# Kernel tuning notes

Measured on AMD Instinct MI355X. Metric: run time of the kernel, lower is better.

The kernel has to match this reference:

```python
import jax, jax.numpy as jnp
import numpy as np

SIGMA = 20.0  # outlier threshold used by FindOutliers
EPS = 1e-8


def setup_inputs() -> dict:
    key = jax.random.key(0)
    k1, k2, k3 = jax.random.split(key, 3)
    B, S, K, N = 2, 2048, 4096, 4096
    x = jax.random.normal(k1, (B, S, K), jnp.float32)
    # inject 8 outlier feature columns (|x| > sigma) so the fp correction path is exercised
    out_cols = jnp.arange(8) * (K // 8)
    x = x.at[:, :, out_cols].multiply(30.0)
    weight = jax.random.normal(k2, (N, K), jnp.float32) * (1.0 / np.sqrt(K))
    bias = jax.random.normal(k3, (N,), jnp.float32) * 0.01
    return {"x": x, "weight": weight, "bias": bias}


def reference(x, weight, bias):
    # x: [B,S,K], weight: [N,K], bias: [N]
    B, S, K = x.shape
    N = weight.shape[0]
    xf = x.reshape(-1, K)  # [M,K]

    # FindOutliers: columns where any activation exceeds sigma (as a fixed-size mask)
    col_mask = jnp.any(jnp.abs(xf) > SIGMA, axis=0)          # [K] bool
    keep = jnp.logical_not(col_mask)

    # weight quantization: zero outlier columns, per-output-row symmetric int8
    w_in = weight * keep[None, :].astype(weight.dtype)        # [N,K]
    q_scale = jnp.max(jnp.abs(w_in), axis=1) / 127.0          # [N]
    q_scale = jnp.maximum(q_scale, EPS)
    q_w = jnp.round(jnp.clip(w_in / q_scale[:, None], -128.0, 127.0)).astype(jnp.int8)

    # per-token (row) activation quantization (FindRowScaleF32)
    row_scale = jnp.max(jnp.abs(xf), axis=1, keepdims=True) / 127.0  # [M,1] fp32
    row_scale = jnp.maximum(row_scale, EPS)
    q_x = jnp.round(jnp.clip(xf / row_scale, -128.0, 127.0)).astype(jnp.int8)

    # int8 GEMM with int32 accumulation, then dequant + bias
    acc = jnp.matmul(q_x.astype(jnp.int32), q_w.T.astype(jnp.int32)).astype(jnp.float32)  # [M,N]
    y = acc * row_scale * q_scale[None, :]

    # fp outlier correction: x[:, ind] @ weight[:, ind].T  (dense masked form, same math)
    x_out = xf * col_mask[None, :].astype(xf.dtype)
    y = y + x_out @ weight.T

    y = y + bias[None, :]
    return y.reshape(B, S, N)
```

## Files before the change

kernel.cpp:

```cpp
#include <hip/hip_runtime.h>
#include <stdint.h>

#define K_DIM 4096
#define N_DIM 4096
#define SIGMA 20.0f
#define EPSQ 1e-8f

typedef __attribute__((ext_vector_type(4))) int i32x4;

#define GLDS16(gp, lp)                                                         \
  __builtin_amdgcn_global_load_lds(                                            \
      (const __attribute__((address_space(1))) unsigned int*)(const void*)(gp),\
      (__attribute__((address_space(3))) unsigned int*)(void*)(lp), 16, 0, 0)

__global__ __launch_bounds__(256) void k_rowquant(
    const float* __restrict__ x, float* __restrict__ row_scale,
    int* __restrict__ mask, int8_t* __restrict__ qx)
{
  const int wave = threadIdx.x >> 6;
  const int lane = threadIdx.x & 63;
  const int m = blockIdx.x * 4 + wave;
  const float4* xr = (const float4*)(x + (size_t)m * K_DIM);
  float4 v[16];
  float amax = 0.0f;
#pragma unroll
  for (int c = 0; c < 16; ++c) {
    v[c] = xr[lane + c * 64];
    float a0 = fabsf(v[c].x), a1 = fabsf(v[c].y);
    float a2 = fabsf(v[c].z), a3 = fabsf(v[c].w);
    amax = fmaxf(amax, fmaxf(fmaxf(a0, a1), fmaxf(a2, a3)));
    int kb = (lane + c * 64) * 4;
    if (a0 > SIGMA) mask[kb + 0] = 1;
    if (a1 > SIGMA) mask[kb + 1] = 1;
    if (a2 > SIGMA) mask[kb + 2] = 1;
    if (a3 > SIGMA) mask[kb + 3] = 1;
  }
#pragma unroll
  for (int off = 32; off > 0; off >>= 1)
    amax = fmaxf(amax, __shfl_xor(amax, off, 64));
  const float rs = fmaxf(amax / 127.0f, EPSQ);
  if (lane == 0) row_scale[m] = rs;
  uint32_t* qxo = (uint32_t*)(qx + (size_t)m * K_DIM);
#pragma unroll
  for (int c = 0; c < 16; ++c) {
    int q0 = (int)rintf(fminf(fmaxf(v[c].x / rs, -128.0f), 127.0f));
    int q1 = (int)rintf(fminf(fmaxf(v[c].y / rs, -128.0f), 127.0f));
    int q2 = (int)rintf(fminf(fmaxf(v[c].z / rs, -128.0f), 127.0f));
    int q3 = (int)rintf(fminf(fmaxf(v[c].w / rs, -128.0f), 127.0f));
    qxo[lane + c * 64] = (uint32_t)(q0 & 0xff) | ((uint32_t)(q1 & 0xff) << 8) |
                         ((uint32_t)(q2 & 0xff) << 16) | ((uint32_t)(q3 & 0xff) << 24);
  }
}

__global__ __launch_bounds__(256) void k_wquant(
    const float* __restrict__ w, const int* __restrict__ mask,
    float* __restrict__ q_scale, int8_t* __restrict__ qw,
    int* __restrict__ outlist, int* __restrict__ count)
{
  if (blockIdx.x == 0) {
    __shared__ int lcnt;
    if (threadIdx.x == 0) lcnt = 0;
    __syncthreads();
    for (int k = threadIdx.x; k < K_DIM; k += 256)
      if (mask[k] == 1) { int i = atomicAdd(&lcnt, 1); outlist[i] = k; }
    __syncthreads();
    if (threadIdx.x == 0) *count = lcnt;
  }

  const int wave = threadIdx.x >> 6;
  const int lane = threadIdx.x & 63;
  const int n = blockIdx.x * 4 + wave;
  const float4* wr = (const float4*)(w + (size_t)n * K_DIM);
  const int4* mr = (const int4*)mask;
  float4 v[16];
  float amax = 0.0f;
#pragma unroll
  for (int c = 0; c < 16; ++c) {
    float4 vv = wr[lane + c * 64];
    int4 mm = mr[lane + c * 64];
    vv.x = (mm.x == 1) ? 0.0f : vv.x;
    vv.y = (mm.y == 1) ? 0.0f : vv.y;
    vv.z = (mm.z == 1) ? 0.0f : vv.z;
    vv.w = (mm.w == 1) ? 0.0f : vv.w;
    v[c] = vv;
    amax = fmaxf(amax, fmaxf(fmaxf(fabsf(vv.x), fabsf(vv.y)),
                             fmaxf(fabsf(vv.z), fabsf(vv.w))));
  }
#pragma unroll
  for (int off = 32; off > 0; off >>= 1)
    amax = fmaxf(amax, __shfl_xor(amax, off, 64));
  const float qs = fmaxf(amax / 127.0f, EPSQ);
  if (lane == 0) q_scale[n] = qs;
  uint32_t* qwo = (uint32_t*)(qw + (size_t)n * K_DIM);
#pragma unroll
  for (int c = 0; c < 16; ++c) {
    int q0 = (int)rintf(fminf(fmaxf(v[c].x / qs, -128.0f), 127.0f));
    int q1 = (int)rintf(fminf(fmaxf(v[c].y / qs, -128.0f), 127.0f));
    int q2 = (int)rintf(fminf(fmaxf(v[c].z / qs, -128.0f), 127.0f));
    int q3 = (int)rintf(fminf(fmaxf(v[c].w / qs, -128.0f), 127.0f));
    qwo[lane + c * 64] = (uint32_t)(q0 & 0xff) | ((uint32_t)(q1 & 0xff) << 8) |
                         ((uint32_t)(q2 & 0xff) << 16) | ((uint32_t)(q3 & 0xff) << 24);
  }
}

__global__ __launch_bounds__(256) void k_gemm(
    const int8_t* __restrict__ qx, const int8_t* __restrict__ qw,
    const float* __restrict__ row_scale, const float* __restrict__ q_scale,
    const float* __restrict__ bias,
    const float* __restrict__ x, const float* __restrict__ w,
    const int* __restrict__ outlist, const int* __restrict__ outcount,
    float* __restrict__ out)
{
  __shared__ int8_t As[128 * 64];
  __shared__ int8_t Bs[128 * 64];
  __shared__ float xsh[128][8];
  __shared__ float wsh[128][8];

  const int t = threadIdx.x;
  const int m0 = blockIdx.y * 128;
  const int n0 = blockIdx.x * 128;

  const int lane = t & 63;
  const int wave = t >> 6;
  const int wm = (wave & 1) * 64;
  const int wn = (wave >> 1) * 64;
  const int lrow = lane & 15;
  const int kg = lane >> 4;

  i32x4 acc[4][4] = {};

  const int srow = t >> 2;
  const int clog = (t & 3) ^ ((t >> 3) & 3);
  const int8_t* gA = qx + (size_t)(m0 + srow) * K_DIM + clog * 16;
  const int8_t* gB = qw + (size_t)(n0 + srow) * K_DIM + clog * 16;

  int offA[4], offB[4];
#pragma unroll
  for (int i = 0; i < 4; ++i) {
    int rA = wm + i * 16 + lrow;
    offA[i] = rA * 64 + ((kg ^ ((rA >> 1) & 3)) * 16);
    int rB = wn + i * 16 + lrow;
    offB[i] = rB * 64 + ((kg ^ ((rB >> 1) & 3)) * 16);
  }

  for (int k0 = 0; k0 < K_DIM; k0 += 64) {
    GLDS16(gA + k0,                        As + t * 16);
    GLDS16(gA + (size_t)64 * K_DIM + k0,   As + 4096 + t * 16);
    GLDS16(gB + k0,                        Bs + t * 16);
    GLDS16(gB + (size_t)64 * K_DIM + k0,   Bs + 4096 + t * 16);
    __syncthreads();

    i32x4 af[4], bf[4];
#pragma unroll
    for (int i = 0; i < 4; ++i) af[i] = *(const i32x4*)(As + offA[i]);
#pragma unroll
    for (int j = 0; j < 4; ++j) bf[j] = *(const i32x4*)(Bs + offB[j]);
#pragma unroll
    for (int i = 0; i < 4; ++i)
#pragma unroll
      for (int j = 0; j < 4; ++j)
        acc[i][j] = __builtin_amdgcn_mfma_i32_16x16x64_i8(af[i], bf[j], acc[i][j], 0, 0, 0);
    __syncthreads();
  }

  const int cnt = *outcount;
  const int cs = cnt < 8 ? cnt : 8;
#pragma unroll
  for (int u = 0; u < 4; ++u) {
    int idx = t * 4 + u;
    int rr = idx >> 3;
    int oo = idx & 7;
    float xv = 0.0f, wv = 0.0f;
    if (oo < cs) {
      int kcol = outlist[oo];
      xv = x[(size_t)(m0 + rr) * K_DIM + kcol];
      wv = w[(size_t)(n0 + rr) * K_DIM + kcol];
    }
    xsh[rr][oo] = xv;
    wsh[rr][oo] = wv;
  }
  __syncthreads();

  float qs[4], bv[4];
  int gn[4];
#pragma unroll
  for (int j = 0; j < 4; ++j) {
    gn[j] = n0 + wn + j * 16 + lrow;
    qs[j] = q_scale[gn[j]];
    bv[j] = bias[gn[j]];
  }

#pragma unroll
  for (int i = 0; i < 4; ++i) {
#pragma unroll
    for (int r = 0; r < 4; ++r) {
      int ml = wm + i * 16 + kg * 4 + r;
      int gm = m0 + ml;
      float rs = row_scale[gm];
      float xvv[8];
#pragma unroll
      for (int o = 0; o < 8; ++o) xvv[o] = xsh[ml][o];
#pragma unroll
      for (int j = 0; j < 4; ++j) {
        int nl = wn + j * 16 + lrow;
        float corr = 0.0f;
#pragma unroll
        for (int o = 0; o < 8; ++o) corr += xvv[o] * wsh[nl][o];
        for (int o = 8; o < cnt; ++o)
          corr += x[(size_t)gm * K_DIM + outlist[o]] *
                  w[(size_t)gn[j] * K_DIM + outlist[o]];
        float val = (float)acc[i][j][r] * rs * qs[j] + corr + bv[j];
        out[(size_t)gm * N_DIM + gn[j]] = val;
      }
    }
  }
}

extern "C" void kernel_launch(void* const* d_in, const int* in_sizes, int n_in,
                              void* d_out, int out_size, void* d_ws, size_t ws_size,
                              hipStream_t stream) {
  const float* x = (const float*)d_in[0];
  const float* w = (const float*)d_in[1];
  const float* bias = (const float*)d_in[2];
  float* out = (float*)d_out;
  const int M = in_sizes[0] / K_DIM;

  char* ws = (char*)d_ws;
  int* mask = (int*)(ws);
  int* count = (int*)(ws + 16384);
  int* outlist = (int*)(ws + 20480);
  float* row_scale = (float*)(ws + 36864);
  float* q_scale = (float*)(ws + 53248);
  int8_t* qx = (int8_t*)(ws + 131072);
  int8_t* qw = (int8_t*)(ws + 131072 + (size_t)M * K_DIM);

  k_rowquant<<<M / 4, 256, 0, stream>>>(x, row_scale, mask, qx);
  k_wquant<<<N_DIM / 4, 256, 0, stream>>>(w, mask, q_scale, qw, outlist, count);
  dim3 grid(N_DIM / 128, M / 128);
  k_gemm<<<grid, dim3(256, 1, 1), 0, stream>>>(qx, qw, row_scale, q_scale, bias,
                                               x, w, outlist, count, out);
}
```

Before: 277.0 us.

## Use single-wave 64x64 GEMM blocks with double-buffered direct-to-LDS loads

The int8 GEMM changes from 256-thread 128x128 blocks to single-wave 64x64 blocks. Each block double-buffers its A/B tiles in LDS, using explicit vmcnt/lgkmcnt waits in place of block-wide barriers, so the loads for step t+2 are issued before the MFMAs of step t. Dropping barriers and overlapping global loads with compute is meant to hide memory latency. The cost is half the data reuse per tile, so twice the global traffic for qx and qw, plus reliance on hand-coded waitcnt encodings being correct for this architecture.

```diff
diff --git a/kernel.cpp b/kernel.cpp
--- a/kernel.cpp
+++ b/kernel.cpp
@@ -12,6 +12,9 @@
   __builtin_amdgcn_global_load_lds(                                            \
       (const __attribute__((address_space(1))) unsigned int*)(const void*)(gp),\
       (__attribute__((address_space(3))) unsigned int*)(void*)(lp), 16, 0, 0)
+
+#define WAITCNT_VM8   0x0F78
+#define WAITCNT_LGKM0 0xC07F
 
 __global__ __launch_bounds__(256) void k_rowquant(
     const float* __restrict__ x, float* __restrict__ row_scale,
@@ -103,7 +106,7 @@
   }
 }
 
-__global__ __launch_bounds__(256) void k_gemm(
+__global__ __launch_bounds__(64, 2) void k_gemm(
     const int8_t* __restrict__ qx, const int8_t* __restrict__ qw,
     const float* __restrict__ row_scale, const float* __restrict__ q_scale,
     const float* __restrict__ bias,
@@ -111,73 +114,83 @@
     const int* __restrict__ outlist, const int* __restrict__ outcount,
     float* __restrict__ out)
 {
-  __shared__ int8_t As[128 * 64];
-  __shared__ int8_t Bs[128 * 64];
-  __shared__ float xsh[128][8];
-  __shared__ float wsh[128][8];
-
-  const int t = threadIdx.x;
-  const int m0 = blockIdx.y * 128;
-  const int n0 = blockIdx.x * 128;
-
-  const int lane = t & 63;
-  const int wave = t >> 6;
-  const int wm = (wave & 1) * 64;
-  const int wn = (wave >> 1) * 64;
+  __shared__ int8_t Abuf[2][64 * 64];
+  __shared__ int8_t Bbuf[2][64 * 64];
+  __shared__ float xsh[64][8];
+  __shared__ float wsh[64][8];
+
+  const int lane = threadIdx.x;
+  const int m0 = blockIdx.y * 64;
+  const int n0 = blockIdx.x * 64;
+
   const int lrow = lane & 15;
   const int kg = lane >> 4;
 
   i32x4 acc[4][4] = {};
 
-  const int srow = t >> 2;
-  const int clog = (t & 3) ^ ((t >> 3) & 3);
+  const int srow = lane >> 2;
+  const int clog = (lane & 3) ^ ((lane >> 3) & 3);
   const int8_t* gA = qx + (size_t)(m0 + srow) * K_DIM + clog * 16;
   const int8_t* gB = qw + (size_t)(n0 + srow) * K_DIM + clog * 16;
 
   int offA[4], offB[4];
 #pragma unroll
   for (int i = 0; i < 4; ++i) {
-    int rA = wm + i * 16 + lrow;
+    int rA = i * 16 + lrow;
     offA[i] = rA * 64 + ((kg ^ ((rA >> 1) & 3)) * 16);
-    int rB = wn + i * 16 + lrow;
+    int rB = i * 16 + lrow;
     offB[i] = rB * 64 + ((kg ^ ((rB >> 1) & 3)) * 16);
   }
 
-  for (int k0 = 0; k0 < K_DIM; k0 += 64) {
-    GLDS16(gA + k0,                        As + t * 16);
-    GLDS16(gA + (size_t)64 * K_DIM + k0,   As + 4096 + t * 16);
-    GLDS16(gB + k0,                        Bs + t * 16);
-    GLDS16(gB + (size_t)64 * K_DIM + k0,   Bs + 4096 + t * 16);
-    __syncthreads();
-
+#define STAGE(buf, k0)                                                        \
+  {                                                                           \
+    _Pragma("unroll")                                                         \
+    for (int i = 0; i < 4; ++i)                                               \
+      GLDS16(gA + (k0) + (size_t)i * 16 * K_DIM,                              \
+             Abuf[buf] + i * 1024 + lane * 16);                               \
+    _Pragma("unroll")                                                         \
+    for (int i = 0; i < 4; ++i)                                               \
+      GLDS16(gB + (k0) + (size_t)i * 16 * K_DIM,                              \
+             Bbuf[buf] + i * 1024 + lane * 16);                               \
+  }
+
+  STAGE(0, 0);
+  STAGE(1, 64);
+
+  for (int t = 0; t < K_DIM / 64; ++t) {
+    const int buf = t & 1;
+    __builtin_amdgcn_s_waitcnt(WAITCNT_VM8);
+    __builtin_amdgcn_sched_barrier(0);
     i32x4 af[4], bf[4];
 #pragma unroll
-    for (int i = 0; i < 4; ++i) af[i] = *(const i32x4*)(As + offA[i]);
-#pragma unroll
-    for (int j = 0; j < 4; ++j) bf[j] = *(const i32x4*)(Bs + offB[j]);
+    for (int i = 0; i < 4; ++i) af[i] = *(const i32x4*)(Abuf[buf] + offA[i]);
+#pragma unroll
+    for (int j = 0; j < 4; ++j) bf[j] = *(const i32x4*)(Bbuf[buf] + offB[j]);
+    __builtin_amdgcn_s_waitcnt(WAITCNT_LGKM0);
+    __builtin_amdgcn_sched_barrier(0);
+    STAGE(buf, ((t + 2) & (K_DIM / 64 - 1)) * 64);
 #pragma unroll
     for (int i = 0; i < 4; ++i)
 #pragma unroll
       for (int j = 0; j < 4; ++j)
         acc[i][j] = __builtin_amdgcn_mfma_i32_16x16x64_i8(af[i], bf[j], acc[i][j], 0, 0, 0);
-    __syncthreads();
-  }
+  }
+#undef STAGE
+
+  __syncthreads();
 
   const int cnt = *outcount;
   const int cs = cnt < 8 ? cnt : 8;
 #pragma unroll
-  for (int u = 0; u < 4; ++u) {
-    int idx = t * 4 + u;
-    int rr = idx >> 3;
-    int oo = idx & 7;
+  for (int o = 0; o < 8; ++o) {
     float xv = 0.0f, wv = 0.0f;
-    if (oo < cs) {
-      int kcol = outlist[oo];
-      xv = x[(size_t)(m0 + rr) * K_DIM + kcol];
-      wv = w[(size_t)(n0 + rr) * K_DIM + kcol];
+    if (o < cs) {
+      int kcol = outlist[o];
+      xv = x[(size_t)(m0 + lane) * K_DIM + kcol];
+      wv = w[(size_t)(n0 + lane) * K_DIM + kcol];
     }
-    xsh[rr][oo] = xv;
-    wsh[rr][oo] = wv;
+    xsh[lane][o] = xv;
+    wsh[lane][o] = wv;
   }
   __syncthreads();
 
@@ -185,7 +198,7 @@
   int gn[4];
 #pragma unroll
   for (int j = 0; j < 4; ++j) {
-    gn[j] = n0 + wn + j * 16 + lrow;
+    gn[j] = n0 + j * 16 + lrow;
     qs[j] = q_scale[gn[j]];
     bv[j] = bias[gn[j]];
   }
@@ -194,7 +207,7 @@
   for (int i = 0; i < 4; ++i) {
 #pragma unroll
     for (int r = 0; r < 4; ++r) {
-      int ml = wm + i * 16 + kg * 4 + r;
+      int ml = i * 16 + kg * 4 + r;
       int gm = m0 + ml;
       float rs = row_scale[gm];
       float xvv[8];
@@ -202,7 +215,7 @@
       for (int o = 0; o < 8; ++o) xvv[o] = xsh[ml][o];
 #pragma unroll
       for (int j = 0; j < 4; ++j) {
-        int nl = wn + j * 16 + lrow;
+        int nl = j * 16 + lrow;
         float corr = 0.0f;
 #pragma unroll
         for (int o = 0; o < 8; ++o) corr += xvv[o] * wsh[nl][o];
@@ -236,7 +249,7 @@
 
   k_rowquant<<<M / 4, 256, 0, stream>>>(x, row_scale, mask, qx);
   k_wquant<<<N_DIM / 4, 256, 0, stream>>>(w, mask, q_scale, qw, outlist, count);
-  dim3 grid(N_DIM / 128, M / 128);
-  k_gemm<<<grid, dim3(256, 1, 1), 0, stream>>>(qx, qw, row_scale, q_scale, bias,
-                                               x, w, outlist, count, out);
-}
+  dim3 grid(N_DIM / 64, M / 64);
+  k_gemm<<<grid, dim3(64, 1, 1), 0, stream>>>(qx, qw, row_scale, q_scale, bias,
+                                              x, w, outlist, count, out);
+}
```

Result: slower. 333.3 us (+20.3%).
